# Performance work log

Hardware: AMD Instinct MI355X
Metric: run time of the kernel (lower is better)

Reference implementation:

```python
import jax, jax.numpy as jnp
import numpy as np


def setup_inputs() -> dict:
    key = jax.random.key(0)
    k1, k2, k3 = jax.random.split(key, 3)
    B, C, H, W = 16, 256, 32, 32
    K, D = 8192, 256
    z = jax.random.normal(k1, (B, C, H, W), dtype=jnp.float32)
    # torch init: uniform(-1/K, 1/K); use small-scale values for realism
    embedding = jax.random.uniform(k2, (K, D), dtype=jnp.float32,
                                   minval=-1.0 / K, maxval=1.0 / K)
    proj_w = jax.random.normal(k3, (D, D), dtype=jnp.float32) * (1.0 / np.sqrt(D))
    return {"z": z, "embedding": embedding, "proj_w": proj_w}


def reference(z, embedding, proj_w):
    commitment_cost = 0.25
    B, C, H, W = z.shape
    # codebook = Linear(embedding) with no bias: emb @ W^T  -> [K, D]
    codebook = embedding @ proj_w.T
    zt = jnp.transpose(z, (0, 2, 3, 1))            # [B, H, W, C]
    zf = zt.reshape(-1, C)                          # [N, C], N = B*H*W
    # squared distances: ||z||^2 + ||e||^2 - 2 z.e  -> [N, K]
    d = (jnp.sum(zf * zf, axis=1, keepdims=True)
         + jnp.sum(codebook * codebook, axis=1)
         - 2.0 * jnp.einsum('nd,kd->nk', zf, codebook))
    min_encoding_indices = jnp.argmin(d, axis=1)    # [N]
    z_quantized = codebook[min_encoding_indices].reshape(zt.shape)  # [B,H,W,C]
    commitment_loss = commitment_cost * jnp.mean(
        (jax.lax.stop_gradient(z_quantized) - zt) ** 2)
    codebook_loss = jnp.mean((z_quantized - jax.lax.stop_gradient(zt)) ** 2)
    loss = commitment_loss + codebook_loss
    # straight-through estimator
    zq_st = zt + jax.lax.stop_gradient(z_quantized - zt)
    out = jnp.transpose(zq_st, (0, 3, 1, 2))        # [B, C, H, W]
    idx = min_encoding_indices.reshape(B, H, W)
    return out, loss, commitment_loss, codebook_loss, idx
```

## Files before the change

kernel.cpp:

```cpp
#include <hip/hip_runtime.h>
#include <cfloat>


constexpr int Dd = 256;
constexpr float INV_M = 1.0f / 4194304.0f;
constexpr float DLT = 8e-4f;
constexpr int SLOTS = 128;

typedef unsigned short u16;
typedef unsigned int u32;
typedef __attribute__((ext_vector_type(8))) short short8;
typedef __attribute__((ext_vector_type(4))) float f32x4;

__device__ __forceinline__ unsigned monof(float f) {
  unsigned u = __float_as_uint(f);
  return (u & 0x80000000u) ? ~u : (u | 0x80000000u);
}
__device__ __forceinline__ float unmonof(unsigned p) {
  unsigned u = (p & 0x80000000u) ? (p & 0x7FFFFFFFu) : ~p;
  return __uint_as_float(u);
}
__device__ __forceinline__ u16 f2bf(float x) {
  unsigned u = __float_as_uint(x);
  u += 0x7FFFu + ((u >> 16) & 1u);
  return (u16)(u >> 16);
}

__global__ __launch_bounds__(256)
void k_codebook(const float* __restrict__ emb, const float* __restrict__ proj,
                float* __restrict__ cb, u16* __restrict__ ef) {
  __shared__ float et[64 * 65];
  __shared__ float pt[64 * 65];
  __shared__ __align__(16) u16 tileT[64 * 72];
  const int t = threadIdx.x;
  const int tx = t & 15, ty = t >> 4;
  const int kb = blockIdx.x * 64;
  const int db = blockIdx.y * 64;
  float acc[4][4];
#pragma unroll
  for (int u = 0; u < 4; ++u)
#pragma unroll
    for (int v = 0; v < 4; ++v) acc[u][v] = 0.f;

  const int jm = t & 15;
  const int q  = t >> 4;

  for (int jc = 0; jc < Dd; jc += 64) {
    __syncthreads();
#pragma unroll
    for (int i = 0; i < 4; ++i) {
      const int row = q + i * 16;
      const float4 e4 = *(const float4*)(emb  + (size_t)(kb + row) * Dd + jc + jm * 4);
      const float4 p4 = *(const float4*)(proj + (size_t)(db + row) * Dd + jc + jm * 4);
      et[(jm*4 + 0) * 65 + row] = e4.x;
      et[(jm*4 + 1) * 65 + row] = e4.y;
      et[(jm*4 + 2) * 65 + row] = e4.z;
      et[(jm*4 + 3) * 65 + row] = e4.w;
      pt[(jm*4 + 0) * 65 + row] = p4.x;
      pt[(jm*4 + 1) * 65 + row] = p4.y;
      pt[(jm*4 + 2) * 65 + row] = p4.z;
      pt[(jm*4 + 3) * 65 + row] = p4.w;
    }
    __syncthreads();
#pragma unroll 16
    for (int j = 0; j < 64; ++j) {
      float a[4], b[4];
#pragma unroll
      for (int u = 0; u < 4; ++u) a[u] = et[j*65 + ty*4 + u];
#pragma unroll
      for (int v = 0; v < 4; ++v) b[v] = pt[j*65 + tx*4 + v];
#pragma unroll
      for (int u = 0; u < 4; ++u)
#pragma unroll
        for (int v = 0; v < 4; ++v) acc[u][v] = fmaf(a[u], b[v], acc[u][v]);
    }
  }
#pragma unroll
  for (int u = 0; u < 4; ++u) {
    const int k = kb + ty*4 + u;
#pragma unroll
    for (int v = 0; v < 4; ++v) {
      const int d = db + tx*4 + v;
      const float val = acc[u][v];
      cb[(size_t)k * Dd + d] = val;
      tileT[(ty*4 + u) * 72 + tx*4 + v] = f2bf(val);
    }
  }
  __syncthreads();
  uint4* ef16 = (uint4*)ef;
#pragma unroll
  for (int w2 = 0; w2 < 2; ++w2) {
    const int uu = w2 * 256 + t;
    const int k16g = uu >> 7;
    const int d32g = (uu >> 6) & 1;
    const int ln   = uu & 63;
    const int klo  = k16g * 16 + (ln & 15);
    const int dlo  = d32g * 32 + (ln >> 4) * 8;
    ef16[((kb >> 4) + k16g) * 512 + ((db >> 5) + d32g) * 64 + ln] =
        *(const uint4*)&tileT[klo * 72 + dlo];
  }
}

__global__ __launch_bounds__(256)
void k_norms(const float* __restrict__ cb, float* __restrict__ norms) {
  const int k = blockIdx.x * 256 + threadIdx.x;
  const float* row = cb + (size_t)k * Dd;
  float s = 0.f;
  for (int d = 0; d < Dd; d += 4) {
    const float4 v = *(const float4*)(row + d);
    s = fmaf(v.x, v.x, s);
    s = fmaf(v.y, v.y, s);
    s = fmaf(v.z, v.z, s);
    s = fmaf(v.w, v.w, s);
  }
  norms[k] = s;
}

__global__ __launch_bounds__(256)
void k_prep_z(const float* __restrict__ z, u16* __restrict__ zf,
              float* __restrict__ znorm) {
  __shared__ float tile[256 * 33];
  const int t = threadIdx.x;
  const int blk = blockIdx.x;
  const int w = t & 31, rg = t >> 5;
  const size_t zbase = (size_t)(blk >> 5) * 262144 + (size_t)(blk & 31) * 32 + w;
#pragma unroll 8
  for (int i = 0; i < 32; ++i) {
    const int d = rg * 32 + i;
    tile[d * 33 + w] = z[zbase + (size_t)d * 1024];
  }
  __syncthreads();
  if (t < 32) {
    float s = 0.f;
    for (int d = 0; d < Dd; ++d) {
      const float v = tile[d * 33 + t];
      s = fmaf(v, v, s);
    }
    znorm[blk * 32 + t] = s;
  }
  const int ml16 = t & 15;
  const int seg  = (t >> 4) & 7;
  const int hi   = t >> 7;
  const int nl   = hi * 16 + ml16;
  uint4* zf16 = (uint4*)zf;
  const int ubase = ((blk * 2 + hi) * 8 + seg) * 64 + ml16;
#pragma unroll
  for (int j = 0; j < 4; ++j) {
    u16 hb[8];
#pragma unroll
    for (int e = 0; e < 8; ++e)
      hb[e] = f2bf(tile[(seg * 32 + j * 8 + e) * 33 + nl]);
    zf16[ubase + j * 16] = *(const uint4*)hb;
  }
}

__global__ __launch_bounds__(256, 2)
void k_scan(const u16* __restrict__ zf, const u16* __restrict__ ef,
            const float* __restrict__ norms, const float* __restrict__ znorm,
            u32* __restrict__ rowminG, u32* __restrict__ rowcnt,
            u32* __restrict__ slots) {
  const int t    = threadIdx.x;
  const int lane = t & 63;
  const int ml   = lane & 15;
  const int qd   = lane >> 4;
  const int wvu  = __builtin_amdgcn_readfirstlane(t >> 6);
  const int rowhalf = wvu & 1;
  const int colhalf = wvu >> 1;
  const int bid  = blockIdx.x;
  const int kb   = (bid & 7) * 1024;
  const int nb   = (bid >> 3) * 64;

  const uint4* zf16 = (const uint4*)zf;
  const uint4* ef16 = (const uint4*)ef;
  const uint4* za = zf16 + (size_t)((nb >> 4) + rowhalf * 2) * 512 + lane;
  const uint4* eb = ef16 + (size_t)((kb >> 4) + colhalf * 8) * 512 + lane;

  float zn[2][4];
#pragma unroll
  for (int rt = 0; rt < 2; ++rt) {
    const int nr = nb + rowhalf * 32 + rt * 16 + qd * 4;
    const f32x4 z4 = *(const f32x4*)(znorm + nr);
#pragma unroll
    for (int r = 0; r < 4; ++r) zn[rt][r] = z4[r];
  }

#pragma unroll 1
  for (int kt = 0; kt < 4; ++kt) {
    const size_t ekt = (size_t)kt * 16 * 512;
#pragma unroll
    for (int cq = 0; cq < 2; ++cq) {
      const uint4* ecq = eb + ekt + (size_t)(cq * 4) * 512;

      f32x4 acc[2][4];
#pragma unroll
      for (int rt = 0; rt < 2; ++rt)
#pragma unroll
        for (int ct = 0; ct < 4; ++ct) acc[rt][ct] = (f32x4)0.f;

      short8 Aa0[2], Aa1[2], Bb0[4], Bb1[4];
#pragma unroll
      for (int rt = 0; rt < 2; ++rt) Aa0[rt] = *(const short8*)(za + rt * 512);
#pragma unroll
      for (int ct = 0; ct < 4; ++ct) Bb0[ct] = *(const short8*)(ecq + ct * 512);

#pragma unroll
      for (int d32 = 0; d32 < 8; ++d32) {
        if (d32 < 7) {
          const int off = (d32 + 1) * 64;
          if (d32 & 1) {
#pragma unroll
            for (int rt = 0; rt < 2; ++rt)
              Aa0[rt] = *(const short8*)(za + rt * 512 + off);
#pragma unroll
            for (int ct = 0; ct < 4; ++ct)
              Bb0[ct] = *(const short8*)(ecq + ct * 512 + off);
          } else {
#pragma unroll
            for (int rt = 0; rt < 2; ++rt)
              Aa1[rt] = *(const short8*)(za + rt * 512 + off);
#pragma unroll
            for (int ct = 0; ct < 4; ++ct)
              Bb1[ct] = *(const short8*)(ecq + ct * 512 + off);
          }
        }
        if (d32 & 1) {
#pragma unroll
          for (int ct = 0; ct < 4; ++ct)
#pragma unroll
            for (int rt = 0; rt < 2; ++rt)
              acc[rt][ct] = __builtin_amdgcn_mfma_f32_16x16x32_bf16(
                  Aa1[rt], Bb1[ct], acc[rt][ct], 0, 0, 0);
        } else {
#pragma unroll
          for (int ct = 0; ct < 4; ++ct)
#pragma unroll
            for (int rt = 0; rt < 2; ++rt)
              acc[rt][ct] = __builtin_amdgcn_mfma_f32_16x16x32_bf16(
                  Aa0[rt], Bb0[ct], acc[rt][ct], 0, 0, 0);
        }
      }

#pragma unroll
      for (int ct = 0; ct < 4; ++ct) {
        const int k0 = kb + kt * 256 + colhalf * 128 + cq * 64 + ct * 16 + ml;
        const float nkv = norms[k0];
#pragma unroll
        for (int rt = 0; rt < 2; ++rt)
#pragma unroll
          for (int r = 0; r < 4; ++r)
            acc[rt][ct][r] = (zn[rt][r] + nkv) - 2.0f * acc[rt][ct][r];
      }

      float m2[2][4];
#pragma unroll
      for (int rt = 0; rt < 2; ++rt)
#pragma unroll
        for (int r = 0; r < 4; ++r) {
          float m = fminf(fminf(acc[rt][0][r], acc[rt][1][r]),
                          fminf(acc[rt][2][r], acc[rt][3][r]));
#pragma unroll
          for (int s = 1; s < 16; s <<= 1) m = fminf(m, __shfl_xor(m, s, 64));
          m2[rt][r] = m;
        }

      unsigned myg = 0xFFFFFFFFu;
      if (ml < 8) {
        const int rt = ml >> 2, r = ml & 3;
        const int n = nb + rowhalf * 32 + rt * 16 + qd * 4 + r;
        const unsigned pk = monof(m2[rt][r]);
        const unsigned old = atomicMin(&rowminG[n], pk);
        myg = min(old, pk);
      }
      float thrv[2][4];
#pragma unroll
      for (int rt = 0; rt < 2; ++rt)
#pragma unroll
        for (int r = 0; r < 4; ++r) {
          const unsigned gg = __shfl(myg, (lane & 48) + rt * 4 + r, 64);
          thrv[rt][r] = unmonof(gg) + DLT;
        }

#pragma unroll
      for (int ct = 0; ct < 4; ++ct) {
        const int k = kb + kt * 256 + colhalf * 128 + cq * 64 + ct * 16 + ml;
#pragma unroll
        for (int rt = 0; rt < 2; ++rt)
#pragma unroll
          for (int r = 0; r < 4; ++r) {
            if (acc[rt][ct][r] <= thrv[rt][r]) {
              const int n = nb + rowhalf * 32 + rt * 16 + qd * 4 + r;
              const u32 pos = atomicAdd(&rowcnt[n], 1u);
              if (pos < (u32)SLOTS) {
                const float e = acc[rt][ct][r] - zn[rt][r];
                int q = __float2int_rn(e * 2097152.0f) + 262144;
                q = q < 0 ? 0 : (q > 524287 ? 524287 : q);
                slots[n * SLOTS + pos] = ((u32)q << 13) | (u32)k;
              }
            }
          }
      }
    }
    __syncthreads();
  }
}

__global__ __launch_bounds__(256)
void k_rescore(const float* __restrict__ z, const float* __restrict__ cb,
               const float* __restrict__ norms, const float* __restrict__ znorm,
               const u32* __restrict__ rowminG, const u32* __restrict__ rowcnt,
               const u32* __restrict__ slots,
               unsigned long long* __restrict__ packed) {
  __shared__ float ztl[32 * 261];
  const int t = threadIdx.x;
  const int blk = blockIdx.x;
  const int w = t & 31, dg = t >> 5;
  const size_t zbase = (size_t)(blk >> 5) * 262144 + (size_t)(blk & 31) * 32;
#pragma unroll 8
  for (int i = 0; i < 32; ++i) {
    const int d = dg * 32 + i;
    ztl[w * 261 + d] = z[zbase + (size_t)d * 1024 + w];
  }
  __syncthreads();

  const int lane = t & 63;
  const int wv = t >> 6;
#pragma unroll 1
  for (int i = 0; i < 8; ++i) {
    const int rl = wv * 8 + i;
    const int n = blk * 32 + rl;
    const u32 cnt = rowcnt[n];
    const float znr = znorm[n];
    const float* zp = ztl + rl * 261 + lane * 4;
    const float g = unmonof(rowminG[n]);
    const int qThr = __float2int_rn((g + DLT - znr) * 2097152.0f) + 262144 + 68;
    unsigned long long best = 0xFFFFFFFFFFFFFFFFull;
    if (cnt <= (u32)SLOTS) {
      for (u32 c = 0; c < cnt; ++c) {
        const u32 v = slots[n * SLOTS + c];
        if ((int)(v >> 13) > qThr) continue;
        const int k = (int)(v & 8191u);
        const float4 c4 = *(const float4*)(cb + (size_t)k * Dd + lane * 4);
        float p = 0.f;
        p = fmaf(zp[0], c4.x, p);
        p = fmaf(zp[1], c4.y, p);
        p = fmaf(zp[2], c4.z, p);
        p = fmaf(zp[3], c4.w, p);
#pragma unroll
        for (int s = 1; s < 64; s <<= 1) p += __shfl_xor(p, s, 64);
        const float sc = (znr + norms[k]) - 2.0f * p;
        const unsigned long long pk =
            ((unsigned long long)monof(sc) << 32) | (unsigned)k;
        if (pk < best) best = pk;
      }
    } else {
      for (int k = 0; k < 8192; ++k) {
        const float4 c4 = *(const float4*)(cb + (size_t)k * Dd + lane * 4);
        float p = 0.f;
        p = fmaf(zp[0], c4.x, p);
        p = fmaf(zp[1], c4.y, p);
        p = fmaf(zp[2], c4.z, p);
        p = fmaf(zp[3], c4.w, p);
#pragma unroll
        for (int s = 1; s < 64; s <<= 1) p += __shfl_xor(p, s, 64);
        const float sc = (znr + norms[k]) - 2.0f * p;
        const unsigned long long pk =
            ((unsigned long long)monof(sc) << 32) | (unsigned)k;
        if (pk < best) best = pk;
      }
    }
    if (lane == 0 && cnt > 0) packed[n] = best;
  }
}

__global__ __launch_bounds__(256)
void k_output(const float* __restrict__ z, const float* __restrict__ cb,
              const unsigned long long* __restrict__ packed,
              float* __restrict__ out, float* __restrict__ idxf,
              float* __restrict__ ssum) {
  __shared__ float zqT[256 * 33];
  __shared__ float part[4];
  const int t = threadIdx.x;
  const int blk = blockIdx.x;
  const int nbase = blk * 32;

  {
    const int nl = t >> 3, m = t & 7;
    const int idx = (int)(packed[nbase + nl] & 0xFFFFFFFFull) & 8191;
    const float* row = cb + (size_t)idx * Dd;
#pragma unroll
    for (int i = 0; i < 8; ++i) {
      const int d0 = m * 4 + i * 32;
      const float4 v = *(const float4*)(row + d0);
      zqT[(d0 + 0) * 33 + nl] = v.x;
      zqT[(d0 + 1) * 33 + nl] = v.y;
      zqT[(d0 + 2) * 33 + nl] = v.z;
      zqT[(d0 + 3) * 33 + nl] = v.w;
    }
    if (t < 32)
      idxf[nbase + t] = (float)(unsigned)(packed[nbase + t] & 0xFFFFFFFFull);
  }
  __syncthreads();

  const int w = t & 31, cg = t >> 5;
  const size_t base = (size_t)(blk >> 5) * 262144 + (size_t)(blk & 31) * 32 + w;
  float local = 0.f;
#pragma unroll
  for (int cc = 0; cc < 32; ++cc) {
    const int c = cg * 32 + cc;
    const float q  = zqT[c * 33 + w];
    const float zv = z[base + (size_t)c * 1024];
    out[base + (size_t)c * 1024] = q;
    const float dd = q - zv;
    local = fmaf(dd, dd, local);
  }
  float v = local;
#pragma unroll
  for (int m = 1; m < 64; m <<= 1) v += __shfl_xor(v, m, 64);
  if ((t & 63) == 0) part[t >> 6] = v;
  __syncthreads();
  if (t == 0) atomicAdd(ssum, part[0] + part[1] + part[2] + part[3]);
}

__global__ void k_final(const float* __restrict__ ssum, float* __restrict__ scal) {
  const float m = *ssum * INV_M;
  scal[0] = 1.25f * m;
  scal[1] = 0.25f * m;
  scal[2] = m;
}

extern "C" void kernel_launch(void* const* d_in, const int* in_sizes, int n_in,
                              void* d_out, int out_size, void* d_ws, size_t ws_size,
                              hipStream_t stream) {
  const float* z    = (const float*)d_in[0];
  const float* emb  = (const float*)d_in[1];
  const float* proj = (const float*)d_in[2];

  float* out  = (float*)d_out;
  float* scal = out + 4194304;
  float* idxf = out + 4194307;

  float* cb    = (float*)d_ws;
  float* norms = cb + 2097152;
  unsigned long long* packed =
      (unsigned long long*)(norms + 8192);
  float* znorm = (float*)(packed + 16384);
  u16* zf = (u16*)(znorm + 16384);
  u16* ef = zf + 4194304;
  u32* rowminG = (u32*)(ef + 2097152);
  u32* rowcnt = rowminG + 16384;
  u32* slots = rowcnt + 16384;
  float* ssum = (float*)(slots + (size_t)16384 * SLOTS);

  hipMemsetAsync(rowminG, 0xFF, 16384 * sizeof(u32), stream);
  hipMemsetAsync(rowcnt, 0, 16384 * sizeof(u32), stream);
  hipMemsetAsync(packed, 0xFF, 16384 * sizeof(unsigned long long), stream);
  hipMemsetAsync(ssum, 0, sizeof(float), stream);

  k_codebook<<<dim3(128, 4), 256, 0, stream>>>(emb, proj, cb, ef);
  k_norms   <<<32, 256, 0, stream>>>(cb, norms);
  k_prep_z  <<<512, 256, 0, stream>>>(z, zf, znorm);
  k_scan    <<<2048, 256, 0, stream>>>(zf, ef, norms, znorm,
                                       rowminG, rowcnt, slots);
  k_rescore <<<512, 256, 0, stream>>>(z, cb, norms, znorm,
                                      rowminG, rowcnt, slots, packed);
  k_output  <<<512, 256, 0, stream>>>(z, cb, packed, out, idxf, ssum);
  k_final   <<<1, 1, 0, stream>>>(ssum, scal);

  (void)in_sizes; (void)n_in; (void)out_size; (void)ws_size;
}
```

Measured before the change: 393.3 us.

## Keep z fragments in registers across scan, prefetch codebook across tiles, vectorize LDS reads

The scan kernel now loads each wave's whole z A-fragment set (2x8 short8) into registers once, instead of reloading it from global memory for every codebook tile. The double-buffered B prefetch is also carried across cq/kt boundaries, so the next tile's first codebook fragment is in flight before the current tile's epilogue. In the codebook kernel the transposed LDS tiles use a stride of 68, which allows float4 reads instead of scalar ones. The trade-off is higher VGPR pressure in the scan kernel under launch_bounds(256,2), which could cause spills or lower occupancy.

Measured after the change: 387.8 us. About the same (-1.4%).

```diff
diff --git a/kernel.cpp b/kernel.cpp
--- a/kernel.cpp
+++ b/kernel.cpp
@@ -29,8 +29,8 @@
 __global__ __launch_bounds__(256)
 void k_codebook(const float* __restrict__ emb, const float* __restrict__ proj,
                 float* __restrict__ cb, u16* __restrict__ ef) {
-  __shared__ float et[64 * 65];
-  __shared__ float pt[64 * 65];
+  __shared__ __align__(16) float et[64 * 68];
+  __shared__ __align__(16) float pt[64 * 68];
   __shared__ __align__(16) u16 tileT[64 * 72];
   const int t = threadIdx.x;
   const int tx = t & 15, ty = t >> 4;
@@ -52,23 +52,22 @@
       const int row = q + i * 16;
       const float4 e4 = *(const float4*)(emb  + (size_t)(kb + row) * Dd + jc + jm * 4);
       const float4 p4 = *(const float4*)(proj + (size_t)(db + row) * Dd + jc + jm * 4);
-      et[(jm*4 + 0) * 65 + row] = e4.x;
-      et[(jm*4 + 1) * 65 + row] = e4.y;
-      et[(jm*4 + 2) * 65 + row] = e4.z;
-      et[(jm*4 + 3) * 65 + row] = e4.w;
-      pt[(jm*4 + 0) * 65 + row] = p4.x;
-      pt[(jm*4 + 1) * 65 + row] = p4.y;
-      pt[(jm*4 + 2) * 65 + row] = p4.z;
-      pt[(jm*4 + 3) * 65 + row] = p4.w;
+      et[(jm*4 + 0) * 68 + row] = e4.x;
+      et[(jm*4 + 1) * 68 + row] = e4.y;
+      et[(jm*4 + 2) * 68 + row] = e4.z;
+      et[(jm*4 + 3) * 68 + row] = e4.w;
+      pt[(jm*4 + 0) * 68 + row] = p4.x;
+      pt[(jm*4 + 1) * 68 + row] = p4.y;
+      pt[(jm*4 + 2) * 68 + row] = p4.z;
+      pt[(jm*4 + 3) * 68 + row] = p4.w;
     }
     __syncthreads();
 #pragma unroll 16
     for (int j = 0; j < 64; ++j) {
-      float a[4], b[4];
-#pragma unroll
-      for (int u = 0; u < 4; ++u) a[u] = et[j*65 + ty*4 + u];
-#pragma unroll
-      for (int v = 0; v < 4; ++v) b[v] = pt[j*65 + tx*4 + v];
+      const float4 a4 = *(const float4*)(et + j * 68 + ty * 4);
+      const float4 b4 = *(const float4*)(pt + j * 68 + tx * 4);
+      const float a[4] = {a4.x, a4.y, a4.z, a4.w};
+      const float b[4] = {b4.x, b4.y, b4.z, b4.w};
 #pragma unroll
       for (int u = 0; u < 4; ++u)
 #pragma unroll
@@ -172,8 +171,17 @@
 
   const uint4* zf16 = (const uint4*)zf;
   const uint4* ef16 = (const uint4*)ef;
-  const uint4* za = zf16 + (size_t)((nb >> 4) + rowhalf * 2) * 512 + lane;
   const uint4* eb = ef16 + (size_t)((kb >> 4) + colhalf * 8) * 512 + lane;
+
+  short8 A[2][8];
+  {
+    const uint4* za = zf16 + (size_t)((nb >> 4) + rowhalf * 2) * 512 + lane;
+#pragma unroll
+    for (int rt = 0; rt < 2; ++rt)
+#pragma unroll
+      for (int d32 = 0; d32 < 8; ++d32)
+        A[rt][d32] = *(const short8*)(za + rt * 512 + d32 * 64);
+  }
 
   float zn[2][4];
 #pragma unroll
@@ -184,6 +192,10 @@
     for (int r = 0; r < 4; ++r) zn[rt][r] = z4[r];
   }
 
+  short8 Bb0[4], Bb1[4];
+#pragma unroll
+  for (int ct = 0; ct < 4; ++ct) Bb0[ct] = *(const short8*)(eb + ct * 512);
+
 #pragma unroll 1
   for (int kt = 0; kt < 4; ++kt) {
     const size_t ekt = (size_t)kt * 16 * 512;
@@ -197,30 +209,26 @@
 #pragma unroll
         for (int ct = 0; ct < 4; ++ct) acc[rt][ct] = (f32x4)0.f;
 
-      short8 Aa0[2], Aa1[2], Bb0[4], Bb1[4];
-#pragma unroll
-      for (int rt = 0; rt < 2; ++rt) Aa0[rt] = *(const short8*)(za + rt * 512);
-#pragma unroll
-      for (int ct = 0; ct < 4; ++ct) Bb0[ct] = *(const short8*)(ecq + ct * 512);
-
 #pragma unroll
       for (int d32 = 0; d32 < 8; ++d32) {
-        if (d32 < 7) {
-          const int off = (d32 + 1) * 64;
+        const bool last = (kt == 3) && (cq == 1) && (d32 == 7);
+        if (!last) {
+          const uint4* pnext;
+          if (d32 < 7) {
+            pnext = ecq + (d32 + 1) * 64;
+          } else if (cq == 0) {
+            pnext = eb + ekt + (size_t)4 * 512;
+          } else {
+            pnext = eb + ekt + (size_t)16 * 512;
+          }
           if (d32 & 1) {
 #pragma unroll
-            for (int rt = 0; rt < 2; ++rt)
-              Aa0[rt] = *(const short8*)(za + rt * 512 + off);
-#pragma unroll
             for (int ct = 0; ct < 4; ++ct)
-              Bb0[ct] = *(const short8*)(ecq + ct * 512 + off);
+              Bb0[ct] = *(const short8*)(pnext + ct * 512);
           } else {
 #pragma unroll
-            for (int rt = 0; rt < 2; ++rt)
-              Aa1[rt] = *(const short8*)(za + rt * 512 + off);
-#pragma unroll
             for (int ct = 0; ct < 4; ++ct)
-              Bb1[ct] = *(const short8*)(ecq + ct * 512 + off);
+              Bb1[ct] = *(const short8*)(pnext + ct * 512);
           }
         }
         if (d32 & 1) {
@@ -229,14 +237,14 @@
 #pragma unroll
             for (int rt = 0; rt < 2; ++rt)
               acc[rt][ct] = __builtin_amdgcn_mfma_f32_16x16x32_bf16(
-                  Aa1[rt], Bb1[ct], acc[rt][ct], 0, 0, 0);
+                  A[rt][d32], Bb1[ct], acc[rt][ct], 0, 0, 0);
         } else {
 #pragma unroll
           for (int ct = 0; ct < 4; ++ct)
 #pragma unroll
             for (int rt = 0; rt < 2; ++rt)
               acc[rt][ct] = __builtin_amdgcn_mfma_f32_16x16x32_bf16(
-                  Aa0[rt], Bb0[ct], acc[rt][ct], 0, 0, 0);
+                  A[rt][d32], Bb0[ct], acc[rt][ct], 0, 0, 0);
         }
       }
 
```
